# Kernel optimization log

Hardware: AMD Instinct MI355X
Metric: run time of the kernel (lower is better)

Reference implementation:

```python
import jax, jax.numpy as jnp
import numpy as np

BN_EPS = 1e-5


def setup_inputs() -> dict:
    key = jax.random.key(0)
    ks = jax.random.split(key, 6)
    B, N, M, C1, C2 = 8, 8192, 2048, 128, 256
    in_ch = C1 + C2  # 384
    return {
        "xyz1": jax.random.uniform(ks[0], (B, N, 3), dtype=jnp.float32),
        "xyz2": jax.random.uniform(ks[1], (B, M, 3), dtype=jnp.float32),
        "features1": jax.random.normal(ks[2], (B, C1, N), dtype=jnp.float32),
        "features2": jax.random.normal(ks[3], (B, C2, M), dtype=jnp.float32),
        # Conv1d(kernel_size=1, bias=False) weights, squeezed to [out, in]
        "conv_w0": jax.random.normal(ks[4], (256, in_ch), dtype=jnp.float32) * 0.05,
        "gamma0": jnp.ones((256,), dtype=jnp.float32),
        "beta0": jnp.zeros((256,), dtype=jnp.float32),
        "conv_w1": jax.random.normal(ks[5], (256, 256), dtype=jnp.float32) * 0.05,
        "gamma1": jnp.ones((256,), dtype=jnp.float32),
        "beta1": jnp.zeros((256,), dtype=jnp.float32),
    }


def _conv_bn_relu(x, w, gamma, beta):
    # 1x1 Conv1d (no bias) == per-point channel matmul: [B,Cin,N] -> [B,Cout,N]
    x = jnp.einsum("oc,bcn->bon", w, x)
    # BatchNorm1d in training mode: batch stats over (B, N), biased variance
    mu = jnp.mean(x, axis=(0, 2), keepdims=True)
    var = jnp.var(x, axis=(0, 2), keepdims=True)
    x = (x - mu) * jax.lax.rsqrt(var + BN_EPS)
    x = x * gamma[None, :, None] + beta[None, :, None]
    return jax.nn.relu(x)


def reference(xyz1, xyz2, features1, features2,
              conv_w0, gamma0, beta0, conv_w1, gamma1, beta1):
    # squared pairwise distances [B, N, M] (broadcast diff reduced over coord dim)
    diff = xyz1[:, :, None, :] - xyz2[:, None, :, :]  # [B,N,M,3]
    dists = jnp.sum(diff * diff, axis=-1)             # [B,N,M]
    idx = jnp.argmin(dists, axis=-1)                  # [B,N] nearest downsampled point

    # per-batch gather: features2[b, :, idx[b]] -> [B, C2, N]
    interp = jax.vmap(lambda f, i: f[:, i])(features2, idx)

    x = jnp.concatenate([features1, interp], axis=1)  # [B, C1+C2, N]
    x = _conv_bn_relu(x, conv_w0, gamma0, beta0)
    x = _conv_bn_relu(x, conv_w1, gamma1, beta1)
    return x
```

## Files before the change

kernel.cpp:

```cpp
#include <hip/hip_runtime.h>
#include <stdint.h>

typedef unsigned short u16;
typedef unsigned int u32;
typedef __attribute__((ext_vector_type(8))) short short8;
typedef __attribute__((ext_vector_type(4))) float floatx4;

#define WVM4 asm volatile("s_waitcnt vmcnt(4)" ::: "memory")
#define WVM2 asm volatile("s_waitcnt vmcnt(2)" ::: "memory")
#define WVM0 asm volatile("s_waitcnt vmcnt(0)" ::: "memory")
#define SCHED0() __builtin_amdgcn_sched_barrier(0)
#define BAR() __builtin_amdgcn_s_barrier()

__device__ __forceinline__ u16 f2b(float f) {
  union { float f; u32 u; } c; c.f = f;
  u32 u = c.u;
  u += 0x7fffu + ((u >> 16) & 1u);
  return (u16)(u >> 16);
}
__device__ __forceinline__ float b2f(u16 h) {
  union { u32 u; float f; } c; c.u = ((u32)h) << 16;
  return c.f;
}

__device__ __forceinline__ void glds16(const void* g, void* l) {
  __builtin_amdgcn_global_load_lds((__attribute__((address_space(1))) void*)g,
                                   (__attribute__((address_space(3))) void*)l, 16, 0, 0);
}

__global__ void prep_all_k(const float* __restrict__ xyz1, const float* __restrict__ xyz2,
                           float2* __restrict__ cand,
                           const float* __restrict__ f1, u16* __restrict__ f1t,
                           const float* __restrict__ f2, u16* __restrict__ f2t,
                           const float* __restrict__ w0, u16* __restrict__ w0b,
                           const float* __restrict__ w1, u16* __restrict__ w1b,
                           float* __restrict__ sums) {
  __shared__ __align__(16) char smem[9216];
  int blk = blockIdx.x, t = threadIdx.x;
  if (blk < 512) {
    float4* s2 = (float4*)smem;
    int nq = blk & 7, mq = (blk >> 3) & 7, b = blk >> 6;
    const float* x2 = xyz2 + ((size_t)b * 2048 + mq * 256) * 3;
    s2[t] = make_float4(x2[t * 3], x2[t * 3 + 1], x2[t * 3 + 2], 0.f);
    __syncthreads();
    int n0 = nq * 1024 + t;
    float px[4], py[4], pz[4];
#pragma unroll
    for (int q = 0; q < 4; q++) {
      const float* p1 = xyz1 + ((size_t)b * 8192 + n0 + q * 256) * 3;
      px[q] = p1[0]; py[q] = p1[1]; pz[q] = p1[2];
    }
    float best[4] = {3.0e38f, 3.0e38f, 3.0e38f, 3.0e38f};
    int bi[4] = {0, 0, 0, 0};
#pragma unroll 4
    for (int m = 0; m < 256; m++) {
      float4 qq = s2[m];
#pragma unroll
      for (int q = 0; q < 4; q++) {
        float dx = px[q] - qq.x, dy = py[q] - qq.y, dz = pz[q] - qq.z;
        float d = fmaf(dz, dz, fmaf(dy, dy, dx * dx));
        bool c = d < best[q];
        best[q] = c ? d : best[q];
        bi[q] = c ? m : bi[q];
      }
    }
#pragma unroll
    for (int q = 0; q < 4; q++) {
      int n = n0 + q * 256;
      cand[(size_t)mq * 65536 + (size_t)b * 8192 + n] =
          make_float2(best[q], __int_as_float(mq * 256 + bi[q]));
    }
  } else if (blk < 3584) {
    const float* in; u16* out; int C, N, bx, by, bz;
    if (blk < 2560) { int rel = blk - 512;  in = f1; out = f1t; C = 128; N = 8192; bx = rel & 127; by = (rel >> 7) & 1; bz = rel >> 8; }
    else            { int rel = blk - 2560; in = f2; out = f2t; C = 256; N = 2048; bx = rel & 31;  by = (rel >> 5) & 3; bz = rel >> 7; }
    u16 (*tile)[72] = (u16(*)[72])smem;
    int c0 = by * 64, n0 = bx * 64;
    const float* src = in + ((size_t)bz * C + c0) * N + n0;
#pragma unroll
    for (int i = 0; i < 4; i++) {
      int id = t + i * 256;
      int c = id >> 4, nq = (id & 15) * 4;
      float4 v = *(const float4*)(src + (size_t)c * N + nq);
      tile[nq + 0][c] = f2b(v.x);
      tile[nq + 1][c] = f2b(v.y);
      tile[nq + 2][c] = f2b(v.z);
      tile[nq + 3][c] = f2b(v.w);
    }
    __syncthreads();
    int n = t >> 2, ch = (t & 3) * 16;
    u16* dst = out + ((size_t)bz * N + n0 + n) * C + c0 + ch;
    *(uint4*)dst = *(const uint4*)&tile[n][ch];
    *(uint4*)(dst + 8) = *(const uint4*)&tile[n][ch + 8];
  } else {
    int rel = blk - 3584;
    int i = rel * 256 + t;
    if (rel < 384) w0b[i] = f2b(w0[i]);
    else { int j = i - 98304; w1b[j] = f2b(w1[j]); }
    if (rel < 4) sums[i] = 0.f;
  }
}

__global__ __launch_bounds__(512, 1) void gemm1_k(const u16* __restrict__ w0b, const u16* __restrict__ f1t,
                                                  const u16* __restrict__ f2t, const float2* __restrict__ cand,
                                                  float* __restrict__ sum0, float* __restrict__ sq0,
                                                  u16* __restrict__ y0) {
  __shared__ u16 Aw[128 * 384];
  __shared__ u16 Bs[3][128 * 64];
  int t = threadIdx.x;
  int bid = blockIdx.x;
  int ohalf = (bid >> 3) & 1;
  int pairidx = (bid & 7) | ((bid >> 4) << 3);
  int o0 = ohalf * 128;
  int lane = t & 63, wave = t >> 6;
  int wrow = (wave >> 2) * 64;
  int wp = (wave & 3) * 32;
  int lr = lane & 15, lq = lane >> 4;
  int srow = lane >> 3;
  int sch = ((lane & 7) ^ srow) * 8;

#pragma unroll
  for (int it = 0; it < 12; it++) {
    u32 off = (u32)it * 8192 + (u32)t * 16;
    int row = off / 768;
    int c16 = (off - row * 768) >> 4;
    glds16(w0b + (size_t)(o0 + row) * 384 + ((c16 ^ (row & 7)) << 3),
           (char*)Aw + (size_t)it * 8192 + (size_t)wave * 1024);
  }

  int gidx[4][2];
#pragma unroll
  for (int s = 0; s < 4; s++) {
    int pt0 = (pairidx * 4 + s) * 128;
#pragma unroll
    for (int i = 0; i < 2; i++) {
      int p = pt0 + (wave * 2 + i) * 8 + srow;
      float bd = 3.0e38f; int bi = 0;
#pragma unroll
      for (int qc = 0; qc < 8; qc++) {
        float2 c = cand[(size_t)qc * 65536 + p];
        if (c.x < bd) { bd = c.x; bi = __float_as_int(c.y); }
      }
      gidx[s][i] = bi;
    }
  }

  float sa[4][4], qa[4][4];
#pragma unroll
  for (int i = 0; i < 4; i++)
#pragma unroll
    for (int r = 0; r < 4; r++) { sa[i][r] = 0.f; qa[i][r] = 0.f; }

  __syncthreads();

  auto stageT = [&](int T) {
    int s2 = T / 6, k = T % 6, buf = T % 3;
    int pt0s = (pairidx * 4 + s2) * 128;
    size_t bb = (size_t)((pt0s >> 13) << 11);
#pragma unroll
    for (int i = 0; i < 2; i++) {
      int row = (wave * 2 + i) * 8 + srow;
      const u16* src;
      if (k < 2) src = f1t + (size_t)(pt0s + row) * 128 + k * 64 + sch;
      else       src = f2t + (bb + gidx[s2][i]) * 256 + (k * 64 - 128) + sch;
      glds16(src, &Bs[buf][(wave * 2 + i) * 512]);
    }
  };

  stageT(0); stageT(1); stageT(2);

#pragma unroll
  for (int s = 0; s < 4; s++) {
    int pt0 = (pairidx * 4 + s) * 128;
    floatx4 zero = {0.f, 0.f, 0.f, 0.f};
    floatx4 acc[4][2];
#pragma unroll
    for (int i = 0; i < 4; i++)
#pragma unroll
      for (int j = 0; j < 2; j++) acc[i][j] = zero;

#pragma unroll
    for (int k = 0; k < 6; k++) {
      int T = s * 6 + k;
      if (T < 22)      { WVM4; }
      else if (T == 22){ WVM2; }
      else             { WVM0; }
      SCHED0();
      BAR();
      SCHED0();
#pragma unroll
      for (int ks = 0; ks < 2; ks++) {
        short8 af[4], bf[2];
#pragma unroll
        for (int i = 0; i < 4; i++) {
          int row = wrow + i * 16 + lr;
          af[i] = *(const short8*)&Aw[row * 384 + (((k * 8 + (ks << 2) + lq) ^ (lr & 7)) << 3)];
        }
#pragma unroll
        for (int j = 0; j < 2; j++) {
          int row = wp + j * 16 + lr;
          bf[j] = *(const short8*)&Bs[T % 3][row * 64 + ((((ks << 2) | lq) ^ (lr & 7)) << 3)];
        }
#pragma unroll
        for (int i = 0; i < 4; i++)
#pragma unroll
          for (int j = 0; j < 2; j++)
            acc[i][j] = __builtin_amdgcn_mfma_f32_16x16x32_bf16(af[i], bf[j], acc[i][j], 0, 0, 0);
      }
      SCHED0();
      BAR();
      SCHED0();
      if (T + 3 < 24) stageT(T + 3);
    }

#pragma unroll
    for (int i = 0; i < 4; i++) {
#pragma unroll
      for (int j = 0; j < 2; j++) {
        int o = o0 + wrow + i * 16 + lq * 4;
        int p = pt0 + wp + j * 16 + lr;
        uint2 pk;
        pk.x = (u32)f2b(acc[i][j][0]) | ((u32)f2b(acc[i][j][1]) << 16);
        pk.y = (u32)f2b(acc[i][j][2]) | ((u32)f2b(acc[i][j][3]) << 16);
        *(uint2*)&y0[(size_t)p * 256 + o] = pk;
      }
#pragma unroll
      for (int r = 0; r < 4; r++) {
        float v0 = acc[i][0][r], v1 = acc[i][1][r];
        sa[i][r] += v0 + v1;
        qa[i][r] += v0 * v0 + v1 * v1;
      }
    }
  }

#pragma unroll
  for (int i = 0; i < 4; i++)
#pragma unroll
    for (int r = 0; r < 4; r++)
#pragma unroll
      for (int m = 8; m >= 1; m >>= 1) {
        sa[i][r] += __shfl_xor(sa[i][r], m);
        qa[i][r] += __shfl_xor(qa[i][r], m);
      }
  __syncthreads();
  float* red = (float*)&Bs[0][0];
  if (t < 256) red[t] = 0.f;
  __syncthreads();
  if (lr == 0) {
#pragma unroll
    for (int i = 0; i < 4; i++)
#pragma unroll
      for (int r = 0; r < 4; r++) {
        int o = wrow + i * 16 + lq * 4 + r;
        atomicAdd(&red[o], sa[i][r]);
        atomicAdd(&red[128 + o], qa[i][r]);
      }
  }
  __syncthreads();
  if (t < 128) {
    atomicAdd(&sum0[o0 + t], red[t]);
    atomicAdd(&sq0[o0 + t], red[128 + t]);
  }
}

__global__ __launch_bounds__(512, 2) void gemm2_k(const u16* __restrict__ w1b, const u16* __restrict__ y0,
                                                  const float* __restrict__ sum0, const float* __restrict__ sq0,
                                                  const float* __restrict__ gamma0, const float* __restrict__ beta0,
                                                  float* __restrict__ sum1, float* __restrict__ sq1,
                                                  u16* __restrict__ y1) {
  __shared__ u16 Aw[128 * 256];
  __shared__ u16 Bs[2][256 * 64];
  __shared__ float ssc[256], ssh[256];
  int t = threadIdx.x;
  int bid = blockIdx.x;
  int ohalf = (bid >> 3) & 1;
  int pairidx = (bid & 7) | ((bid >> 4) << 3);
  int o0 = ohalf * 128;
  int lane = t & 63, wave = t >> 6;
  int wrow = (wave >> 2) * 64;
  int wp = (wave & 3) * 64;
  int lr = lane & 15, lq = lane >> 4;
  if (t < 256) {
    float mean = sum0[t] * (1.f / 65536.f);
    float var = fmaxf(sq0[t] * (1.f / 65536.f) - mean * mean, 0.f);
    float r = rsqrtf(var + 1e-5f);
    float sc = gamma0[t] * r;
    ssc[t] = sc;
    ssh[t] = beta0[t] - mean * sc;
  }
#pragma unroll
  for (int it = 0; it < 8; it++) {
    u32 off = (u32)it * 8192 + (u32)t * 16;
    int row = off >> 9;
    int c16 = (off & 511) >> 4;
    glds16(w1b + (size_t)(o0 + row) * 256 + ((c16 ^ (row & 7)) << 3),
           (char*)Aw + (size_t)it * 8192 + (size_t)wave * 1024);
  }

  int brow[4], bpc[4], bch[4];
#pragma unroll
  for (int i = 0; i < 4; i++) {
    int id = t + i * 512;
    brow[i] = id >> 3; bpc[i] = id & 7;
    bch[i] = (bpc[i] ^ (brow[i] & 7)) * 8;
  }
  float sa[4][4], qa[4][4];
#pragma unroll
  for (int i = 0; i < 4; i++)
#pragma unroll
    for (int r = 0; r < 4; r++) { sa[i][r] = 0.f; qa[i][r] = 0.f; }

  __syncthreads();

  for (int s = 0; s < 2; s++) {
    int pt0 = (pairidx * 2 + s) * 256;
    uint4 rg[4];
    auto loadB = [&](int k0) {
#pragma unroll
      for (int i = 0; i < 4; i++)
        rg[i] = *(const uint4*)(y0 + (size_t)(pt0 + brow[i]) * 256 + k0 + bch[i]);
    };
    auto xformB = [&](int k0, int bufi) {
#pragma unroll
      for (int i = 0; i < 4; i++) {
        u32 rw[4] = {rg[i].x, rg[i].y, rg[i].z, rg[i].w};
        u32 ow[4];
#pragma unroll
        for (int w = 0; w < 4; w++) {
          int k = k0 + bch[i] + w * 2;
          float v0 = b2f((u16)(rw[w] & 0xffffu));
          float v1 = b2f((u16)(rw[w] >> 16));
          v0 = fmaxf(v0 * ssc[k] + ssh[k], 0.f);
          v1 = fmaxf(v1 * ssc[k + 1] + ssh[k + 1], 0.f);
          ow[w] = (u32)f2b(v0) | ((u32)f2b(v1) << 16);
        }
        uint4 ov; ov.x = ow[0]; ov.y = ow[1]; ov.z = ow[2]; ov.w = ow[3];
        *(uint4*)&Bs[bufi][brow[i] * 64 + bpc[i] * 8] = ov;
      }
    };
    floatx4 zero = {0.f, 0.f, 0.f, 0.f};
    floatx4 acc[4][4];
#pragma unroll
    for (int i = 0; i < 4; i++)
#pragma unroll
      for (int j = 0; j < 4; j++) acc[i][j] = zero;
    auto compute = [&](int k0, int bufi) {
#pragma unroll
      for (int ks = 0; ks < 2; ks++) {
        short8 af[4], bf[4];
#pragma unroll
        for (int i = 0; i < 4; i++) {
          int row = wrow + i * 16 + lr;
          af[i] = *(const short8*)&Aw[row * 256 + ((((k0 >> 3) + (ks << 2) + lq) ^ (lr & 7)) << 3)];
        }
#pragma unroll
        for (int j = 0; j < 4; j++) {
          int row = wp + j * 16 + lr;
          bf[j] = *(const short8*)&Bs[bufi][row * 64 + ((((ks << 2) | lq) ^ (lr & 7)) << 3)];
        }
#pragma unroll
        for (int i = 0; i < 4; i++)
#pragma unroll
          for (int j = 0; j < 4; j++)
            acc[i][j] = __builtin_amdgcn_mfma_f32_16x16x32_bf16(af[i], bf[j], acc[i][j], 0, 0, 0);
      }
    };

    loadB(0);
    xformB(0, 0);
    __syncthreads();
#pragma unroll
    for (int k0i = 0; k0i < 4; k0i++) {
      if (k0i < 3) loadB((k0i + 1) * 64);
      compute(k0i * 64, k0i & 1);
      __syncthreads();
      if (k0i < 3) {
        xformB((k0i + 1) * 64, (k0i + 1) & 1);
        __syncthreads();
      }
    }
#pragma unroll
    for (int i = 0; i < 4; i++) {
#pragma unroll
      for (int j = 0; j < 4; j++) {
        int o = o0 + wrow + i * 16 + lq * 4;
        int p = pt0 + wp + j * 16 + lr;
        uint2 pk;
        pk.x = (u32)f2b(acc[i][j][0]) | ((u32)f2b(acc[i][j][1]) << 16);
        pk.y = (u32)f2b(acc[i][j][2]) | ((u32)f2b(acc[i][j][3]) << 16);
        *(uint2*)&y1[(size_t)p * 256 + o] = pk;
      }
#pragma unroll
      for (int r = 0; r < 4; r++) {
        float v0 = acc[i][0][r], v1 = acc[i][1][r], v2 = acc[i][2][r], v3 = acc[i][3][r];
        sa[i][r] += v0 + v1 + v2 + v3;
        qa[i][r] += v0 * v0 + v1 * v1 + v2 * v2 + v3 * v3;
      }
    }
  }

#pragma unroll
  for (int i = 0; i < 4; i++)
#pragma unroll
    for (int r = 0; r < 4; r++)
#pragma unroll
      for (int m = 8; m >= 1; m >>= 1) {
        sa[i][r] += __shfl_xor(sa[i][r], m);
        qa[i][r] += __shfl_xor(qa[i][r], m);
      }
  __syncthreads();
  float* red = (float*)&Bs[0][0];
  if (t < 256) red[t] = 0.f;
  __syncthreads();
  if (lr == 0) {
#pragma unroll
    for (int i = 0; i < 4; i++)
#pragma unroll
      for (int r = 0; r < 4; r++) {
        int o = wrow + i * 16 + lq * 4 + r;
        atomicAdd(&red[o], sa[i][r]);
        atomicAdd(&red[128 + o], qa[i][r]);
      }
  }
  __syncthreads();
  if (t < 128) {
    atomicAdd(&sum1[o0 + t], red[t]);
    atomicAdd(&sq1[o0 + t], red[128 + t]);
  }
}

__global__ void finalize_k(const u16* __restrict__ y1, const float* __restrict__ sum1,
                           const float* __restrict__ sq1, const float* __restrict__ gamma1,
                           const float* __restrict__ beta1, float* __restrict__ out) {
  __shared__ float tile[64][65];
  __shared__ float fs[64], fh[64];
  int b = blockIdx.z, o0 = blockIdx.y * 64, n0 = blockIdx.x * 64;
  int t = threadIdx.x;
  if (t < 64) {
    int o = o0 + t;
    float mean = sum1[o] * (1.f / 65536.f);
    float var = fmaxf(sq1[o] * (1.f / 65536.f) - mean * mean, 0.f);
    float r = rsqrtf(var + 1e-5f);
    float sc = gamma1[o] * r;
    fs[t] = sc;
    fh[t] = beta1[o] - mean * sc;
  }
  __syncthreads();
  int pl = t >> 2, ch = (t & 3) * 16;
  const u16* src = y1 + ((size_t)(b * 8192 + n0 + pl)) * 256 + o0 + ch;
  uint4 r0 = *(const uint4*)src;
  uint4 r1 = *(const uint4*)(src + 8);
  u16 hv[16];
  *(uint4*)&hv[0] = r0;
  *(uint4*)&hv[8] = r1;
#pragma unroll
  for (int e = 0; e < 16; e++) {
    float v = b2f(hv[e]) * fs[ch + e] + fh[ch + e];
    tile[pl][ch + e] = fmaxf(v, 0.f);
  }
  __syncthreads();
  int ol = t >> 2, nch = (t & 3) * 16;
  float* dst = out + ((size_t)(b * 256 + o0 + ol)) * 8192 + n0 + nch;
#pragma unroll
  for (int j = 0; j < 16; j += 4) {
    float4 v = make_float4(tile[nch + j][ol], tile[nch + j + 1][ol],
                           tile[nch + j + 2][ol], tile[nch + j + 3][ol]);
    *(float4*)(dst + j) = v;
  }
}

extern "C" void kernel_launch(void* const* d_in, const int* in_sizes, int n_in,
                              void* d_out, int out_size, void* d_ws, size_t ws_size,
                              hipStream_t stream) {
  const float* xyz1      = (const float*)d_in[0];
  const float* xyz2      = (const float*)d_in[1];
  const float* features1 = (const float*)d_in[2];
  const float* features2 = (const float*)d_in[3];
  const float* conv_w0   = (const float*)d_in[4];
  const float* gamma0    = (const float*)d_in[5];
  const float* beta0     = (const float*)d_in[6];
  const float* conv_w1   = (const float*)d_in[7];
  const float* gamma1    = (const float*)d_in[8];
  const float* beta1     = (const float*)d_in[9];
  float* out = (float*)d_out;

  char* ws = (char*)d_ws;
  size_t off = 0;
  auto alloc = [&](size_t bytes) {
    char* p = ws + off;
    off = (off + bytes + 4095) & ~(size_t)4095;
    return p;
  };
  float*  sums = (float*)alloc(4 * 256 * 4);
  u16*    w0b  = (u16*)alloc(256 * 384 * 2);
  u16*    w1b  = (u16*)alloc(256 * 256 * 2);
  float2* cand = (float2*)alloc((size_t)8 * 65536 * 8);
  u16*    f1t  = (u16*)alloc((size_t)65536 * 128 * 2);
  u16*    f2t  = (u16*)alloc((size_t)16384 * 256 * 2);
  u16*    y0   = (u16*)alloc((size_t)65536 * 256 * 2);
  u16*    y1   = (u16*)alloc((size_t)65536 * 256 * 2);

  prep_all_k<<<dim3(4224), 256, 0, stream>>>(xyz1, xyz2, cand, features1, f1t,
                                             features2, f2t, conv_w0, w0b, conv_w1, w1b, sums);
  gemm1_k<<<dim3(256), 512, 0, stream>>>(w0b, f1t, f2t, cand, sums + 0, sums + 256, y0);
  gemm2_k<<<dim3(256), 512, 0, stream>>>(w1b, y0, sums + 0, sums + 256, gamma0, beta0,
                                         sums + 512, sums + 768, y1);
  finalize_k<<<dim3(128, 4, 8), 256, 0, stream>>>(y1, sums + 512, sums + 768, gamma1, beta1, out);
}
```

Baseline: 231.4 us.

## Double-buffer B registers in gemm2 to overlap transform with MFMA compute

gemm2 now uses two register buffers for the B-tile loads. Each step applies the BN1 scale, shift and ReLU to the next tile and writes it to the other shared-memory buffer in the same barrier phase as the MFMA compute on the current tile. This cuts the barriers per point tile from seven to four and lets global loads, the transform and the matrix math overlap. The launch bound drops to one block per CU, which frees registers for the extra buffer; shared-memory use likely already limited occupancy to one block. The risk is more register pressure and an extra barrier at the end of each tile.

```diff
diff --git a/kernel.cpp b/kernel.cpp
--- a/kernel.cpp
+++ b/kernel.cpp
@@ -263,7 +263,7 @@
   }
 }
 
-__global__ __launch_bounds__(512, 2) void gemm2_k(const u16* __restrict__ w1b, const u16* __restrict__ y0,
+__global__ __launch_bounds__(512, 1) void gemm2_k(const u16* __restrict__ w1b, const u16* __restrict__ y0,
                                                   const float* __restrict__ sum0, const float* __restrict__ sq0,
                                                   const float* __restrict__ gamma0, const float* __restrict__ beta0,
                                                   float* __restrict__ sum1, float* __restrict__ sq1,
@@ -312,73 +312,78 @@
 
   __syncthreads();
 
+  uint4 rg0[4], rg1[4];
+  auto loadB = [&](int pt0, int k0, uint4* rg) {
+#pragma unroll
+    for (int i = 0; i < 4; i++)
+      rg[i] = *(const uint4*)(y0 + (size_t)(pt0 + brow[i]) * 256 + k0 + bch[i]);
+  };
+  auto xformB = [&](int k0, const uint4* rg, int bufi) {
+#pragma unroll
+    for (int i = 0; i < 4; i++) {
+      u32 rw[4] = {rg[i].x, rg[i].y, rg[i].z, rg[i].w};
+      u32 ow[4];
+#pragma unroll
+      for (int w = 0; w < 4; w++) {
+        int k = k0 + bch[i] + w * 2;
+        float v0 = b2f((u16)(rw[w] & 0xffffu));
+        float v1 = b2f((u16)(rw[w] >> 16));
+        v0 = fmaxf(v0 * ssc[k] + ssh[k], 0.f);
+        v1 = fmaxf(v1 * ssc[k + 1] + ssh[k + 1], 0.f);
+        ow[w] = (u32)f2b(v0) | ((u32)f2b(v1) << 16);
+      }
+      uint4 ov; ov.x = ow[0]; ov.y = ow[1]; ov.z = ow[2]; ov.w = ow[3];
+      *(uint4*)&Bs[bufi][brow[i] * 64 + bpc[i] * 8] = ov;
+    }
+  };
+  floatx4 acc[4][4];
+  auto compute = [&](int k0, int bufi) {
+#pragma unroll
+    for (int ks = 0; ks < 2; ks++) {
+      short8 af[4], bf[4];
+#pragma unroll
+      for (int i = 0; i < 4; i++) {
+        int row = wrow + i * 16 + lr;
+        af[i] = *(const short8*)&Aw[row * 256 + ((((k0 >> 3) + (ks << 2) + lq) ^ (lr & 7)) << 3)];
+      }
+#pragma unroll
+      for (int j = 0; j < 4; j++) {
+        int row = wp + j * 16 + lr;
+        bf[j] = *(const short8*)&Bs[bufi][row * 64 + ((((ks << 2) | lq) ^ (lr & 7)) << 3)];
+      }
+#pragma unroll
+      for (int i = 0; i < 4; i++)
+#pragma unroll
+        for (int j = 0; j < 4; j++)
+          acc[i][j] = __builtin_amdgcn_mfma_f32_16x16x32_bf16(af[i], bf[j], acc[i][j], 0, 0, 0);
+    }
+  };
+
   for (int s = 0; s < 2; s++) {
     int pt0 = (pairidx * 2 + s) * 256;
-    uint4 rg[4];
-    auto loadB = [&](int k0) {
-#pragma unroll
-      for (int i = 0; i < 4; i++)
-        rg[i] = *(const uint4*)(y0 + (size_t)(pt0 + brow[i]) * 256 + k0 + bch[i]);
-    };
-    auto xformB = [&](int k0, int bufi) {
-#pragma unroll
-      for (int i = 0; i < 4; i++) {
-        u32 rw[4] = {rg[i].x, rg[i].y, rg[i].z, rg[i].w};
-        u32 ow[4];
-#pragma unroll
-        for (int w = 0; w < 4; w++) {
-          int k = k0 + bch[i] + w * 2;
-          float v0 = b2f((u16)(rw[w] & 0xffffu));
-          float v1 = b2f((u16)(rw[w] >> 16));
-          v0 = fmaxf(v0 * ssc[k] + ssh[k], 0.f);
-          v1 = fmaxf(v1 * ssc[k + 1] + ssh[k + 1], 0.f);
-          ow[w] = (u32)f2b(v0) | ((u32)f2b(v1) << 16);
-        }
-        uint4 ov; ov.x = ow[0]; ov.y = ow[1]; ov.z = ow[2]; ov.w = ow[3];
-        *(uint4*)&Bs[bufi][brow[i] * 64 + bpc[i] * 8] = ov;
-      }
-    };
     floatx4 zero = {0.f, 0.f, 0.f, 0.f};
-    floatx4 acc[4][4];
 #pragma unroll
     for (int i = 0; i < 4; i++)
 #pragma unroll
       for (int j = 0; j < 4; j++) acc[i][j] = zero;
-    auto compute = [&](int k0, int bufi) {
-#pragma unroll
-      for (int ks = 0; ks < 2; ks++) {
-        short8 af[4], bf[4];
-#pragma unroll
-        for (int i = 0; i < 4; i++) {
-          int row = wrow + i * 16 + lr;
-          af[i] = *(const short8*)&Aw[row * 256 + ((((k0 >> 3) + (ks << 2) + lq) ^ (lr & 7)) << 3)];
-        }
-#pragma unroll
-        for (int j = 0; j < 4; j++) {
-          int row = wp + j * 16 + lr;
-          bf[j] = *(const short8*)&Bs[bufi][row * 64 + ((((ks << 2) | lq) ^ (lr & 7)) << 3)];
-        }
-#pragma unroll
-        for (int i = 0; i < 4; i++)
-#pragma unroll
-          for (int j = 0; j < 4; j++)
-            acc[i][j] = __builtin_amdgcn_mfma_f32_16x16x32_bf16(af[i], bf[j], acc[i][j], 0, 0, 0);
-      }
-    };
-
-    loadB(0);
-    xformB(0, 0);
-    __syncthreads();
-#pragma unroll
-    for (int k0i = 0; k0i < 4; k0i++) {
-      if (k0i < 3) loadB((k0i + 1) * 64);
-      compute(k0i * 64, k0i & 1);
-      __syncthreads();
-      if (k0i < 3) {
-        xformB((k0i + 1) * 64, (k0i + 1) & 1);
-        __syncthreads();
-      }
-    }
+
+    loadB(pt0, 0, rg0);
+    xformB(0, rg0, 0);
+    loadB(pt0, 64, rg1);
+    __syncthreads();
+    loadB(pt0, 128, rg0);
+    xformB(64, rg1, 1);
+    compute(0, 0);
+    __syncthreads();
+    loadB(pt0, 192, rg1);
+    xformB(128, rg0, 0);
+    compute(64, 1);
+    __syncthreads();
+    xformB(192, rg1, 1);
+    compute(128, 0);
+    __syncthreads();
+    compute(192, 1);
+
 #pragma unroll
     for (int i = 0; i < 4; i++) {
 #pragma unroll
@@ -397,6 +402,7 @@
         qa[i][r] += v0 * v0 + v1 * v1 + v2 * v2 + v3 * v3;
       }
     }
+    __syncthreads();
   }
 
 #pragma unroll
```

After: 231.7 us. About the same (+0.2%).
